# Kernel optimization log

Hardware: AMD Instinct MI355X
Metric: run time of the kernel (lower is better)

The kernel has to match this reference:

```python
import jax, jax.numpy as jnp
import numpy as np

N_NODES = 100000
N_EDGES = 3200000
D_IN = 128
D_HID = 16
N_CLS = 2


def gcn_conv(x, edge_index, W, b, n_nodes):
    """PyG GCNConv (normalize=True, add_self_loops=True, bias=True)."""
    h = x @ W  # [N, out]
    loop = jnp.arange(n_nodes, dtype=edge_index.dtype)
    src = jnp.concatenate([edge_index[0], loop])
    dst = jnp.concatenate([edge_index[1], loop])
    deg = jax.ops.segment_sum(jnp.ones_like(dst, dtype=h.dtype), dst, num_segments=n_nodes)
    dinv = jnp.where(deg > 0, jax.lax.rsqrt(deg), jnp.zeros_like(deg))
    norm = dinv[src] * dinv[dst]  # [E+N]
    msg = h[src] * norm[:, None]  # gather + scale
    out = jax.ops.segment_sum(msg, dst, num_segments=n_nodes)  # scatter-add
    return out + b


def setup_inputs() -> dict:
    key = jax.random.key(0)
    k1, k2, k3, k4, k5 = jax.random.split(key, 5)
    x = jax.random.normal(k1, (N_NODES, D_IN), dtype=jnp.float32)
    edge_index = jax.random.randint(k2, (2, N_EDGES), 0, N_NODES, dtype=jnp.int64)
    # Glorot-style init for GCNConv weights, zeros for bias (PyG default)
    W1 = jax.random.normal(k3, (D_IN, D_HID), dtype=jnp.float32) * (1.0 / np.sqrt(D_IN))
    b1 = jnp.zeros((D_HID,), dtype=jnp.float32)
    W2 = jax.random.normal(k4, (D_HID, N_CLS), dtype=jnp.float32) * (1.0 / np.sqrt(D_HID))
    b2 = jnp.zeros((N_CLS,), dtype=jnp.float32)
    return {"x": x, "edge_index": edge_index, "W1": W1, "b1": b1, "W2": W2, "b2": b2}


def reference(x, edge_index, W1, b1, W2, b2):
    n = x.shape[0]
    h = gcn_conv(x, edge_index, W1, b1, n)
    h = jax.nn.relu(h)
    # dropout is identity in eval mode
    h = gcn_conv(h, edge_index, W2, b2, n)
    return jax.nn.log_softmax(h, axis=1)
```

## Files before the change

kernel.cpp:

```cpp
#include <hip/hip_runtime.h>
#include <hip/hip_bf16.h>
#include <hip/hip_fp16.h>

#define D_IN  128
#define D_HID 16
#define N_CLS 2
#define NPB   256
#define MAXB  512
#define TILE  8192
#define XROW  136
#define LCAP  10496

#define FE 0

typedef short bf16x8 __attribute__((ext_vector_type(8)));
typedef float f32x4  __attribute__((ext_vector_type(4)));

__device__ __forceinline__ unsigned short f2bf(float f) {
    unsigned int u = __float_as_uint(f);
    u += 0x7FFFu + ((u >> 16) & 1u);
    return (unsigned short)(u >> 16);
}

template<bool I64>
__device__ __forceinline__ int lde(const void* p, size_t i) {
    if constexpr (I64) return (int)((const long long*)p)[i];
    else               return ((const int*)p)[i];
}

__global__ void k_detect(const int* __restrict__ ev, int* __restrict__ flags) {
    __shared__ int sE;
    if (threadIdx.x == 0) sE = 0;
    __syncthreads();
    if (ev[2 * threadIdx.x + 1] != 0) atomicOr(&sE, 1);
    __syncthreads();
    if (threadIdx.x == 0) flags[FE] = sE ? 0 : 1;
}

template<bool I64>
__device__ __forceinline__ void part_body(
        const void* __restrict__ ei, unsigned int* __restrict__ gcur,
        unsigned int* __restrict__ staged, int E, int cap,
        unsigned int* sbuf, unsigned short* bbuf,
        int* hist, int* lbase, int* gb, int* wsum) {
    int tid = threadIdx.x;
    int t0 = blockIdx.x * TILE;

    if (tid < MAXB) hist[tid] = 0;
    __syncthreads();

    int myB[8]; unsigned int myP[8]; int myR[8];
#pragma unroll
    for (int k = 0; k < 8; ++k) {
        int e = t0 + k * 1024 + tid;
        if (e < E) {
            int s = lde<I64>(ei, (size_t)e);
            int d = lde<I64>(ei, (size_t)E + e);
            int b = d >> 8;
            myB[k] = b;
            myP[k] = ((unsigned int)s << 8) | (unsigned int)(d & 255);
            myR[k] = atomicAdd(&hist[b], 1);
        } else myB[k] = -1;
    }
    __syncthreads();

    int lane = tid & 63, wv = tid >> 6;
    int v = 0, s = 0;
    if (tid < MAXB) {
        v = hist[tid];
        s = v;
#pragma unroll
        for (int m = 1; m < 64; m <<= 1) {
            int t = __shfl_up(s, m, 64);
            if (lane >= m) s += t;
        }
        if (lane == 63) wsum[wv] = s;
    }
    __syncthreads();
    if (tid < MAXB) {
        int woff = 0;
#pragma unroll
        for (int w = 0; w < 8; ++w) if (w < wv) woff += wsum[w];
        int excl = s + woff - v;
        lbase[tid] = excl;
        int gb_ = 0;
        if (v > 0) gb_ = (int)atomicAdd(&gcur[tid], (unsigned int)v);
        gb[tid] = gb_;
    }
    __syncthreads();

#pragma unroll
    for (int k = 0; k < 8; ++k) {
        if (myB[k] >= 0) {
            int pos = lbase[myB[k]] + myR[k];
            sbuf[pos] = myP[k];
            bbuf[pos] = (unsigned short)myB[k];
        }
    }
    __syncthreads();

    int tot = lbase[MAXB - 1] + hist[MAXB - 1];
    for (int i = tid; i < tot; i += 1024) {
        int b = bbuf[i];
        int rel = gb[b] + (i - lbase[b]);
        if (rel < cap)
            staged[(size_t)b * cap + rel] = sbuf[i];
    }
}

__global__ __launch_bounds__(1024) void k_part(
        const void* __restrict__ ei, unsigned int* __restrict__ gcur,
        unsigned int* __restrict__ staged, int E, int cap) {
    __shared__ unsigned int sbuf[TILE];
    __shared__ unsigned short bbuf[TILE];
    __shared__ int hist[MAXB], lbase[MAXB], gb[MAXB];
    __shared__ int wsum[8];
    __shared__ int sI64;
    int tid = threadIdx.x;
    if (tid == 0) sI64 = 1;
    __syncthreads();
    if (tid < 256 && 2 * tid + 1 < 2 * E && ((const int*)ei)[2 * tid + 1] != 0) sI64 = 0;
    __syncthreads();
    if (sI64) part_body<true >(ei, gcur, staged, E, cap, sbuf, bbuf, hist, lbase, gb, wsum);
    else      part_body<false>(ei, gcur, staged, E, cap, sbuf, bbuf, hist, lbase, gb, wsum);
}

__global__ __launch_bounds__(1024) void k_sortd(
        const unsigned int* __restrict__ staged, const unsigned int* __restrict__ gcur,
        unsigned int* __restrict__ staged2, unsigned int* __restrict__ dmeta,
        float* __restrict__ dinv, int cap, int N) {
    __shared__ unsigned int ebuf[LCAP];
    __shared__ unsigned int h[NPB];
    __shared__ unsigned int cur[NPB];
    __shared__ int wsum[4];
    int tid = threadIdx.x, b = blockIdx.x;
    long long s0 = (long long)b * cap;
    int cnt = (int)gcur[b];
    if (cnt > cap - NPB) cnt = cap - NPB;
    bool inL = cnt <= LCAP;
    if (tid < NPB) h[tid] = 0u;
    __syncthreads();
    for (int i = tid; i < cnt; i += 1024) {
        unsigned int p = staged[s0 + i];
        if (inL) ebuf[i] = p;
        atomicAdd(&h[p & 255], 1u);
    }
    __syncthreads();
    int v = 0, sIncl = 0;
    int lane = tid & 63, wv = tid >> 6;
    if (tid < NPB) {
        v = (int)h[tid];
        sIncl = v;
#pragma unroll
        for (int m = 1; m < 64; m <<= 1) {
            int t = __shfl_up(sIncl, m, 64);
            if (lane >= m) sIncl += t;
        }
        if (lane == 63) wsum[wv] = sIncl;
    }
    __syncthreads();
    if (tid < NPB) {
        int woff = 0;
#pragma unroll
        for (int w = 0; w < 4; ++w) if (w < wv) woff += wsum[w];
        int excl = sIncl + woff - v;
        int node = b * NPB + tid;
        int start = excl + tid;
        dmeta[node] = ((unsigned int)start << 16) | (unsigned int)v;
        cur[tid] = (unsigned int)start;
        if (node < N) dinv[node] = rsqrtf((float)(v + 1));
    }
    __syncthreads();
    for (int i = tid; i < cnt; i += 1024) {
        unsigned int p = inL ? ebuf[i] : staged[s0 + i];
        unsigned int r = atomicAdd(&cur[p & 255], 1u);
        staged2[s0 + r] = p;
    }
    __syncthreads();
    if (tid < NPB) {
        unsigned int pos = cur[tid];
        int node = b * NPB + tid;
        if ((int)pos < cap)
            staged2[s0 + pos] = ((unsigned int)node << 8) | (unsigned int)tid;
    }
}

__global__ __launch_bounds__(256) void k_gemm1m(
        const float* __restrict__ x, const float* __restrict__ W1,
        const float* __restrict__ dinv, __half* __restrict__ g1h, int n) {
    __shared__ short xhi[64 * XROW];
    __shared__ short xlo[64 * XROW];
    __shared__ short whi[16 * XROW];
    __shared__ short wlo[16 * XROW];
    int tid = threadIdx.x;
    int node0 = blockIdx.x * 64;

    for (int i = tid; i < D_IN * D_HID; i += 256) {
        int k = i >> 4, f = i & 15;
        float v = W1[i];
        unsigned short h = f2bf(v);
        float fh = __uint_as_float(((unsigned int)h) << 16);
        whi[f * XROW + k] = (short)h;
        wlo[f * XROW + k] = (short)f2bf(v - fh);
    }
    int limFlat = (n - node0) * D_IN;
#pragma unroll
    for (int it = 0; it < 8; ++it) {
        int flat = it * 1024 + tid * 4;
        float4 v = make_float4(0.f, 0.f, 0.f, 0.f);
        if (flat < limFlat) v = *(const float4*)(x + (size_t)node0 * D_IN + flat);
        int row = flat >> 7, k = flat & 127;
        unsigned int u0 = __float_as_uint(v.x), u1 = __float_as_uint(v.y);
        unsigned int u2 = __float_as_uint(v.z), u3 = __float_as_uint(v.w);
        unsigned short l0 = f2bf(v.x - __uint_as_float(u0 & 0xFFFF0000u));
        unsigned short l1 = f2bf(v.y - __uint_as_float(u1 & 0xFFFF0000u));
        unsigned short l2 = f2bf(v.z - __uint_as_float(u2 & 0xFFFF0000u));
        unsigned short l3 = f2bf(v.w - __uint_as_float(u3 & 0xFFFF0000u));
        int o = row * XROW + k;
        *(uint2*)(&xhi[o]) = make_uint2((u0 >> 16) | (u1 & 0xFFFF0000u),
                                        (u2 >> 16) | (u3 & 0xFFFF0000u));
        *(uint2*)(&xlo[o]) = make_uint2((unsigned int)l0 | ((unsigned int)l1 << 16),
                                        (unsigned int)l2 | ((unsigned int)l3 << 16));
    }
    __syncthreads();

    int w = tid >> 6, L = tid & 63;
    int m = L & 15, q = L >> 4;
    const short* axh = &xhi[(w * 16 + m) * XROW + q * 8];
    const short* axl = &xlo[(w * 16 + m) * XROW + q * 8];
    const short* bwh = &whi[m * XROW + q * 8];
    const short* bwl = &wlo[m * XROW + q * 8];
    f32x4 acc = {0.f, 0.f, 0.f, 0.f};
#pragma unroll
    for (int c = 0; c < 4; ++c) {
        bf16x8 ah = *(const bf16x8*)(axh + c * 32);
        bf16x8 al = *(const bf16x8*)(axl + c * 32);
        bf16x8 bh = *(const bf16x8*)(bwh + c * 32);
        bf16x8 bl = *(const bf16x8*)(bwl + c * 32);
        acc = __builtin_amdgcn_mfma_f32_16x16x32_bf16(ah, bh, acc, 0, 0, 0);
        acc = __builtin_amdgcn_mfma_f32_16x16x32_bf16(ah, bl, acc, 0, 0, 0);
        acc = __builtin_amdgcn_mfma_f32_16x16x32_bf16(al, bh, acc, 0, 0, 0);
    }
    int nodeB = node0 + w * 16 + q * 4;
#pragma unroll
    for (int r = 0; r < 4; ++r) {
        int node = nodeB + r;
        if (node < n) g1h[(size_t)node * D_HID + m] = __float2half(dinv[node] * acc[r]);
    }
}

__global__ __launch_bounds__(256) void k_agg1w(
        const unsigned int* __restrict__ staged2, const unsigned int* __restrict__ dmeta,
        const __half* __restrict__ g1h,
        const float* __restrict__ b1, const float* __restrict__ W2,
        float2* __restrict__ g2, int N, int cap) {
    int tid = threadIdx.x, b = blockIdx.x, by = blockIdx.y;
    long long s0 = (long long)b * cap;
    int lane = tid & 63;
    int f2 = lane & 7;
    int e8 = lane >> 3;
    int wid = (by << 2) + (tid >> 6);
    const __half2* g1h2 = (const __half2*)g1h;
    int f0 = f2 * 2;
    float b10 = b1[f0], b11 = b1[f0 + 1];
    float w00 = W2[f0 * N_CLS + 0], w01 = W2[f0 * N_CLS + 1];
    float w10 = W2[(f0 + 1) * N_CLS + 0], w11 = W2[(f0 + 1) * N_CLS + 1];
    unsigned int md[8];
#pragma unroll
    for (int k = 0; k < 8; ++k) md[k] = dmeta[b * NPB + wid + (k << 5)];
#pragma unroll 4
    for (int k = 0; k < 8; ++k) {
        int node = b * NPB + wid + (k << 5);
        const unsigned int* sp = staged2 + s0 + (md[k] >> 16);
        int cnt = (int)(md[k] & 0xFFFFu) + 1;
        float ax = 0.f, ay = 0.f;
        for (int base = 0; base < cnt; base += 64) {
            unsigned int pe[8];
#pragma unroll
            for (int j = 0; j < 8; ++j) {
                int idx = base + (j << 3) + e8;
                int c = idx < cnt ? idx : cnt - 1;
                pe[j] = sp[c];
            }
#pragma unroll
            for (int j = 0; j < 8; ++j) {
                int idx = base + (j << 3) + e8;
                float2 t = __half22float2(g1h2[(size_t)(pe[j] >> 8) * 8 + f2]);
                if (idx < cnt) { ax += t.x; ay += t.y; }
            }
        }
        ax += __shfl_xor(ax, 8, 64);  ay += __shfl_xor(ay, 8, 64);
        ax += __shfl_xor(ax, 16, 64); ay += __shfl_xor(ay, 16, 64);
        ax += __shfl_xor(ax, 32, 64); ay += __shfl_xor(ay, 32, 64);
        float di = rsqrtf((float)cnt);
        float r0 = fmaxf(b10 + di * ax, 0.f);
        float r1 = fmaxf(b11 + di * ay, 0.f);
        float c0 = r0 * w00 + r1 * w10;
        float c1 = r0 * w01 + r1 * w11;
        c0 += __shfl_xor(c0, 1, 64); c1 += __shfl_xor(c1, 1, 64);
        c0 += __shfl_xor(c0, 2, 64); c1 += __shfl_xor(c1, 2, 64);
        c0 += __shfl_xor(c0, 4, 64); c1 += __shfl_xor(c1, 4, 64);
        if (lane == 0 && node < N) g2[node] = make_float2(di * c0, di * c1);
    }
}

__global__ __launch_bounds__(256) void k_agg2w(
        const unsigned int* __restrict__ staged2, const unsigned int* __restrict__ dmeta,
        const float2* __restrict__ g2,
        const float* __restrict__ b2, float2* __restrict__ out, int N, int cap) {
    int tid = threadIdx.x, b = blockIdx.x, by = blockIdx.y;
    long long s0 = (long long)b * cap;
    int lane = tid & 63;
    int wid = (by << 2) + (tid >> 6);
    float bb0 = b2[0], bb1 = b2[1];
    unsigned int md[8];
#pragma unroll
    for (int k = 0; k < 8; ++k) md[k] = dmeta[b * NPB + wid + (k << 5)];
#pragma unroll 4
    for (int k = 0; k < 8; ++k) {
        int node = b * NPB + wid + (k << 5);
        const unsigned int* sp = staged2 + s0 + (md[k] >> 16);
        int cnt = (int)(md[k] & 0xFFFFu) + 1;
        float a0 = 0.f, a1 = 0.f;
        for (int base = 0; base < cnt; base += 64) {
            int idx = base + lane;
            int c = idx < cnt ? idx : cnt - 1;
            unsigned int p = sp[c];
            float2 t = g2[p >> 8];
            if (idx < cnt) { a0 += t.x; a1 += t.y; }
        }
#pragma unroll
        for (int mm = 1; mm < 64; mm <<= 1) {
            a0 += __shfl_xor(a0, mm, 64);
            a1 += __shfl_xor(a1, mm, 64);
        }
        if (lane == 0 && node < N) {
            float di = rsqrtf((float)cnt);
            float v0 = bb0 + di * a0;
            float v1 = bb1 + di * a1;
            float mx = fmaxf(v0, v1);
            float lse = mx + logf(expf(v0 - mx) + expf(v1 - mx));
            out[node] = make_float2(v0 - lse, v1 - lse);
        }
    }
}

__global__ void fb_deg_init(unsigned int* __restrict__ deg, int n) {
    int i = blockIdx.x * blockDim.x + threadIdx.x;
    if (i < n) deg[i] = 1u;
}
template<bool I64>
__global__ void fb_deg_count(const void* __restrict__ ei, unsigned int* __restrict__ deg,
                             int E, const int* __restrict__ flags) {
    if (flags[FE] != (int)I64) return;
    int e = blockIdx.x * blockDim.x + threadIdx.x;
    if (e < E) atomicAdd(&deg[lde<I64>(ei, (size_t)E + e)], 1u);
}
__global__ void fb_dinv_inplace(float* __restrict__ dinv, int n) {
    int i = blockIdx.x * blockDim.x + threadIdx.x;
    if (i < n) {
        unsigned int u = ((const unsigned int*)dinv)[i];
        dinv[i] = rsqrtf((float)u);
    }
}
__global__ void fb_a1_init(const float* __restrict__ h1, const float* __restrict__ dinv,
                           const float* __restrict__ b1, float* __restrict__ a1, int n) {
    int tid = blockIdx.x * blockDim.x + threadIdx.x;
    if (tid >= n * D_HID) return;
    int node = tid >> 4, f = tid & 15;
    float di = dinv[node];
    a1[tid] = b1[f] + di * di * h1[tid];
}
template<bool I64>
__global__ void fb_agg1(const void* __restrict__ ei, const float* __restrict__ dinv,
                        const float* __restrict__ h1, float* __restrict__ a1,
                        int E, const int* __restrict__ flags) {
    if (flags[FE] != (int)I64) return;
    int tid = blockIdx.x * blockDim.x + threadIdx.x;
    int e = tid >> 4, f = tid & 15;
    if (e >= E) return;
    int s = lde<I64>(ei, (size_t)e);
    int d = lde<I64>(ei, (size_t)E + e);
    float norm = dinv[s] * dinv[d];
    atomicAdd(&a1[(size_t)d * D_HID + f], h1[(size_t)s * D_HID + f] * norm);
}
__global__ void fb_relu_gemm2(const float* __restrict__ a1, const float* __restrict__ W2,
                              float* __restrict__ h2, int n) {
    int node = blockIdx.x * blockDim.x + threadIdx.x;
    if (node >= n) return;
    float c0 = 0.f, c1 = 0.f;
    const float* row = a1 + (size_t)node * D_HID;
#pragma unroll
    for (int f = 0; f < D_HID; ++f) {
        float r = fmaxf(row[f], 0.f);
        c0 += r * W2[f * N_CLS + 0];
        c1 += r * W2[f * N_CLS + 1];
    }
    h2[(size_t)node * 2 + 0] = c0;
    h2[(size_t)node * 2 + 1] = c1;
}
__global__ void fb_a2_init(const float* __restrict__ h2, const float* __restrict__ dinv,
                           const float* __restrict__ b2, float* __restrict__ a2, int n) {
    int tid = blockIdx.x * blockDim.x + threadIdx.x;
    if (tid >= n * N_CLS) return;
    int node = tid >> 1, c = tid & 1;
    float di = dinv[node];
    a2[tid] = b2[c] + di * di * h2[tid];
}
template<bool I64>
__global__ void fb_agg2(const void* __restrict__ ei, const float* __restrict__ dinv,
                        const float* __restrict__ h2, float* __restrict__ a2,
                        int E, const int* __restrict__ flags) {
    if (flags[FE] != (int)I64) return;
    int e = blockIdx.x * blockDim.x + threadIdx.x;
    if (e >= E) return;
    int s = lde<I64>(ei, (size_t)e);
    int d = lde<I64>(ei, (size_t)E + e);
    float norm = dinv[s] * dinv[d];
    atomicAdd(&a2[(size_t)d * 2 + 0], h2[(size_t)s * 2 + 0] * norm);
    atomicAdd(&a2[(size_t)d * 2 + 1], h2[(size_t)s * 2 + 1] * norm);
}
__global__ void fb_gemm1(const float* __restrict__ x, const float* __restrict__ W1,
                         float* __restrict__ h1, int n) {
    __shared__ float w[D_IN * D_HID];
    for (int i = threadIdx.x; i < D_IN * D_HID; i += blockDim.x) w[i] = W1[i];
    __syncthreads();
    int tid = blockIdx.x * blockDim.x + threadIdx.x;
    int node = tid >> 4, f = tid & 15;
    if (node >= n) return;
    const float4* xr = (const float4*)(x + (size_t)node * D_IN);
    float acc = 0.f;
#pragma unroll
    for (int k4 = 0; k4 < D_IN / 4; ++k4) {
        float4 v = xr[k4];
        int k = k4 * 4;
        acc += v.x * w[(k + 0) * D_HID + f];
        acc += v.y * w[(k + 1) * D_HID + f];
        acc += v.z * w[(k + 2) * D_HID + f];
        acc += v.w * w[(k + 3) * D_HID + f];
    }
    h1[tid] = acc;
}
__global__ void fb_lsm(const float* __restrict__ a2, float* __restrict__ out, int n) {
    int node = blockIdx.x * blockDim.x + threadIdx.x;
    if (node >= n) return;
    float v0 = a2[(size_t)node * 2 + 0];
    float v1 = a2[(size_t)node * 2 + 1];
    float m = fmaxf(v0, v1);
    float lse = m + logf(expf(v0 - m) + expf(v1 - m));
    out[(size_t)node * 2 + 0] = v0 - lse;
    out[(size_t)node * 2 + 1] = v1 - lse;
}

extern "C" void kernel_launch(void* const* d_in, const int* in_sizes, int n_in,
                              void* d_out, int out_size, void* d_ws, size_t ws_size,
                              hipStream_t stream) {
    const float* x  = (const float*)d_in[0];
    const void*  ei = d_in[1];
    const float* W1 = (const float*)d_in[2];
    const float* b1 = (const float*)d_in[3];
    const float* W2 = (const float*)d_in[4];
    const float* b2 = (const float*)d_in[5];

    const int N = in_sizes[0] / D_IN;
    const int E = in_sizes[1] / 2;
    const int nb = (N + NPB - 1) / NPB;

    int cap = ((2 * (E / nb + 1) + NPB) + 255) & ~255;
    if (cap < 1024) cap = 1024;

    const int B = 256;
    dim3 blk(B);
    const int nBlkN = (N + B - 1) / B;
    const int nBlkE = (E + B - 1) / B;
    char* ws = (char*)d_ws;

    auto al = [](size_t v) { return (v + 255) & ~(size_t)255; };
    const size_t oDinv   = 0;
    const size_t oDmeta  = al(oDinv + (size_t)N * 4);
    const size_t oGcur   = al(oDmeta + (size_t)nb * NPB * 4);
    const size_t oFlag   = al(oGcur + (size_t)MAXB * 4);
    const size_t oStage  = al(oFlag + 8);
    const size_t oStage2 = al(oStage + (size_t)nb * cap * 4);
    const size_t oG1h    = al(oStage2 + (size_t)nb * cap * 4);
    const size_t oG2     = al(oG1h + (size_t)N * D_HID * 2);
    const size_t needNew = al(oG2 + (size_t)N * 2 * 4);

    if (ws_size >= needNew && nb <= MAXB && cap <= 65280 && N < (1 << 24) - NPB) {
        float*        dinv    = (float*)(ws + oDinv);
        unsigned int* dmeta   = (unsigned int*)(ws + oDmeta);
        unsigned int* gcur    = (unsigned int*)(ws + oGcur);
        unsigned int* staged  = (unsigned int*)(ws + oStage);
        unsigned int* staged2 = (unsigned int*)(ws + oStage2);
        __half*       g1h     = (__half*)(ws + oG1h);
        float2*       g2      = (float2*)(ws + oG2);

        hipMemsetAsync(gcur, 0, (size_t)nb * 4, stream);

        dim3 gPart((E + TILE - 1) / TILE);
        k_part<<<gPart, dim3(1024), 0, stream>>>(ei, gcur, staged, E, cap);

        k_sortd<<<dim3(nb), dim3(1024), 0, stream>>>(staged, gcur, staged2, dmeta, dinv, cap, N);

        k_gemm1m<<<dim3((N + 63) / 64), dim3(256), 0, stream>>>(x, W1, dinv, g1h, N);

        k_agg1w<<<dim3(nb, 8), dim3(256), 0, stream>>>(staged2, dmeta, g1h, b1, W2, g2, N, cap);

        k_agg2w<<<dim3(nb, 8), dim3(256), 0, stream>>>(staged2, dmeta, g2, b2,
                                                       (float2*)d_out, N, cap);
    } else {
        float* dinv  = (float*)(ws + 0);
        float* h1    = (float*)(ws + 400128);
        float* a1    = (float*)(ws + 6800256);
        float* h2    = (float*)(ws + 13200384);
        float* a2    = (float*)(ws + 14000512);
        int*   flags = (int*)  (ws + 14800640);

        k_detect<<<dim3(1), blk, 0, stream>>>((const int*)ei, flags);
        fb_deg_init<<<dim3(nBlkN), blk, 0, stream>>>((unsigned int*)dinv, N);
        fb_deg_count<false><<<dim3(nBlkE), blk, 0, stream>>>(ei, (unsigned int*)dinv, E, flags);
        fb_deg_count<true ><<<dim3(nBlkE), blk, 0, stream>>>(ei, (unsigned int*)dinv, E, flags);
        fb_dinv_inplace<<<dim3(nBlkN), blk, 0, stream>>>(dinv, N);

        dim3 g_nh((N * D_HID + B - 1) / B);
        fb_gemm1<<<g_nh, blk, 0, stream>>>(x, W1, h1, N);
        fb_a1_init<<<g_nh, blk, 0, stream>>>(h1, dinv, b1, a1, N);
        dim3 g_eh(((size_t)E * D_HID + B - 1) / B);
        fb_agg1<false><<<g_eh, blk, 0, stream>>>(ei, dinv, h1, a1, E, flags);
        fb_agg1<true ><<<g_eh, blk, 0, stream>>>(ei, dinv, h1, a1, E, flags);
        fb_relu_gemm2<<<dim3(nBlkN), blk, 0, stream>>>(a1, W2, h2, N);
        dim3 g_n2((N * N_CLS + B - 1) / B);
        fb_a2_init<<<g_n2, blk, 0, stream>>>(h2, dinv, b2, a2, N);
        fb_agg2<false><<<dim3(nBlkE), blk, 0, stream>>>(ei, dinv, h2, a2, E, flags);
        fb_agg2<true ><<<dim3(nBlkE), blk, 0, stream>>>(ei, dinv, h2, a2, E, flags);
        fb_lsm<<<dim3(nBlkN), blk, 0, stream>>>(a2, (float*)d_out, N);
    }
}
```

Measured before the change: 213.0 us.

## Fuse per-bucket sort into layer-1 aggregation and count degrees in partition

Removes the separate k_sortd kernel. Degree counting moves into the partition kernel as global atomics on a zeroed deg array, and the GEMM computes dinv from it. The bucket counting sort and the layer-1 aggregation are fused into one 1024-thread block per bucket, which reads the sorted edges from LDS. This saves a launch and a pass over the staged edges. In exchange it adds 3.2M global atomics, and the aggregation runs with only nb blocks instead of nb×8, which lowers parallelism.

```diff
diff --git a/kernel.cpp b/kernel.cpp
--- a/kernel.cpp
+++ b/kernel.cpp
@@ -40,7 +40,8 @@
 template<bool I64>
 __device__ __forceinline__ void part_body(
         const void* __restrict__ ei, unsigned int* __restrict__ gcur,
-        unsigned int* __restrict__ staged, int E, int cap,
+        unsigned int* __restrict__ staged, unsigned int* __restrict__ deg,
+        int E, int cap,
         unsigned int* sbuf, unsigned short* bbuf,
         int* hist, int* lbase, int* gb, int* wsum) {
     int tid = threadIdx.x;
@@ -60,6 +61,7 @@
             myB[k] = b;
             myP[k] = ((unsigned int)s << 8) | (unsigned int)(d & 255);
             myR[k] = atomicAdd(&hist[b], 1);
+            atomicAdd(&deg[d], 1u);
         } else myB[k] = -1;
     }
     __syncthreads();
@@ -110,7 +112,8 @@
 
 __global__ __launch_bounds__(1024) void k_part(
         const void* __restrict__ ei, unsigned int* __restrict__ gcur,
-        unsigned int* __restrict__ staged, int E, int cap) {
+        unsigned int* __restrict__ staged, unsigned int* __restrict__ deg,
+        int E, int cap) {
     __shared__ unsigned int sbuf[TILE];
     __shared__ unsigned short bbuf[TILE];
     __shared__ int hist[MAXB], lbase[MAXB], gb[MAXB];
@@ -121,73 +124,13 @@
     __syncthreads();
     if (tid < 256 && 2 * tid + 1 < 2 * E && ((const int*)ei)[2 * tid + 1] != 0) sI64 = 0;
     __syncthreads();
-    if (sI64) part_body<true >(ei, gcur, staged, E, cap, sbuf, bbuf, hist, lbase, gb, wsum);
-    else      part_body<false>(ei, gcur, staged, E, cap, sbuf, bbuf, hist, lbase, gb, wsum);
-}
-
-__global__ __launch_bounds__(1024) void k_sortd(
-        const unsigned int* __restrict__ staged, const unsigned int* __restrict__ gcur,
-        unsigned int* __restrict__ staged2, unsigned int* __restrict__ dmeta,
-        float* __restrict__ dinv, int cap, int N) {
-    __shared__ unsigned int ebuf[LCAP];
-    __shared__ unsigned int h[NPB];
-    __shared__ unsigned int cur[NPB];
-    __shared__ int wsum[4];
-    int tid = threadIdx.x, b = blockIdx.x;
-    long long s0 = (long long)b * cap;
-    int cnt = (int)gcur[b];
-    if (cnt > cap - NPB) cnt = cap - NPB;
-    bool inL = cnt <= LCAP;
-    if (tid < NPB) h[tid] = 0u;
-    __syncthreads();
-    for (int i = tid; i < cnt; i += 1024) {
-        unsigned int p = staged[s0 + i];
-        if (inL) ebuf[i] = p;
-        atomicAdd(&h[p & 255], 1u);
-    }
-    __syncthreads();
-    int v = 0, sIncl = 0;
-    int lane = tid & 63, wv = tid >> 6;
-    if (tid < NPB) {
-        v = (int)h[tid];
-        sIncl = v;
-#pragma unroll
-        for (int m = 1; m < 64; m <<= 1) {
-            int t = __shfl_up(sIncl, m, 64);
-            if (lane >= m) sIncl += t;
-        }
-        if (lane == 63) wsum[wv] = sIncl;
-    }
-    __syncthreads();
-    if (tid < NPB) {
-        int woff = 0;
-#pragma unroll
-        for (int w = 0; w < 4; ++w) if (w < wv) woff += wsum[w];
-        int excl = sIncl + woff - v;
-        int node = b * NPB + tid;
-        int start = excl + tid;
-        dmeta[node] = ((unsigned int)start << 16) | (unsigned int)v;
-        cur[tid] = (unsigned int)start;
-        if (node < N) dinv[node] = rsqrtf((float)(v + 1));
-    }
-    __syncthreads();
-    for (int i = tid; i < cnt; i += 1024) {
-        unsigned int p = inL ? ebuf[i] : staged[s0 + i];
-        unsigned int r = atomicAdd(&cur[p & 255], 1u);
-        staged2[s0 + r] = p;
-    }
-    __syncthreads();
-    if (tid < NPB) {
-        unsigned int pos = cur[tid];
-        int node = b * NPB + tid;
-        if ((int)pos < cap)
-            staged2[s0 + pos] = ((unsigned int)node << 8) | (unsigned int)tid;
-    }
+    if (sI64) part_body<true >(ei, gcur, staged, deg, E, cap, sbuf, bbuf, hist, lbase, gb, wsum);
+    else      part_body<false>(ei, gcur, staged, deg, E, cap, sbuf, bbuf, hist, lbase, gb, wsum);
 }
 
 __global__ __launch_bounds__(256) void k_gemm1m(
         const float* __restrict__ x, const float* __restrict__ W1,
-        const float* __restrict__ dinv, __half* __restrict__ g1h, int n) {
+        const unsigned int* __restrict__ deg, __half* __restrict__ g1h, int n) {
     __shared__ short xhi[64 * XROW];
     __shared__ short xlo[64 * XROW];
     __shared__ short whi[16 * XROW];
@@ -245,54 +188,107 @@
 #pragma unroll
     for (int r = 0; r < 4; ++r) {
         int node = nodeB + r;
-        if (node < n) g1h[(size_t)node * D_HID + m] = __float2half(dinv[node] * acc[r]);
-    }
-}
-
-__global__ __launch_bounds__(256) void k_agg1w(
-        const unsigned int* __restrict__ staged2, const unsigned int* __restrict__ dmeta,
+        if (node < n) {
+            float di = rsqrtf((float)(deg[node] + 1u));
+            g1h[(size_t)node * D_HID + m] = __float2half(di * acc[r]);
+        }
+    }
+}
+
+__global__ __launch_bounds__(1024) void k_sagg1(
+        const unsigned int* __restrict__ staged, const unsigned int* __restrict__ gcur,
+        unsigned int* __restrict__ staged2, unsigned int* __restrict__ dmeta,
         const __half* __restrict__ g1h,
         const float* __restrict__ b1, const float* __restrict__ W2,
         float2* __restrict__ g2, int N, int cap) {
-    int tid = threadIdx.x, b = blockIdx.x, by = blockIdx.y;
+    __shared__ unsigned int ebuf[LCAP];
+    __shared__ unsigned int md[NPB];
+    __shared__ unsigned int cur[NPB];
+    __shared__ int wsum[4];
+    int tid = threadIdx.x, b = blockIdx.x;
     long long s0 = (long long)b * cap;
-    int lane = tid & 63;
-    int f2 = lane & 7;
-    int e8 = lane >> 3;
-    int wid = (by << 2) + (tid >> 6);
+    int cnt = (int)gcur[b];
+    if (cnt > cap - NPB) cnt = cap - NPB;
+    bool inL = (cnt + NPB) <= LCAP;
+
+    if (tid < NPB) cur[tid] = 0u;
+    __syncthreads();
+    for (int i = tid; i < cnt; i += 1024)
+        atomicAdd(&cur[staged[s0 + i] & 255], 1u);
+    __syncthreads();
+    int lane = tid & 63, wv = tid >> 6;
+    int v = 0, sIncl = 0;
+    if (tid < NPB) {
+        v = (int)cur[tid];
+        sIncl = v;
+#pragma unroll
+        for (int m = 1; m < 64; m <<= 1) {
+            int t = __shfl_up(sIncl, m, 64);
+            if (lane >= m) sIncl += t;
+        }
+        if (lane == 63) wsum[wv] = sIncl;
+    }
+    __syncthreads();
+    if (tid < NPB) {
+        int woff = 0;
+#pragma unroll
+        for (int w = 0; w < 4; ++w) if (w < wv) woff += wsum[w];
+        int start = (sIncl + woff - v) + tid;
+        md[tid] = ((unsigned int)start << 16) | (unsigned int)v;
+        cur[tid] = (unsigned int)start;
+    }
+    __syncthreads();
+    for (int i = tid; i < cnt; i += 1024) {
+        unsigned int p = staged[s0 + i];
+        unsigned int r = atomicAdd(&cur[p & 255], 1u);
+        staged2[s0 + r] = p;
+        if (inL) ebuf[r] = p;
+    }
+    __syncthreads();
+    if (tid < NPB) {
+        unsigned int pos = cur[tid];
+        int node = b * NPB + tid;
+        dmeta[node] = md[tid];
+        unsigned int sv = ((unsigned int)node << 8) | (unsigned int)tid;
+        if ((int)pos < cap) {
+            staged2[s0 + pos] = sv;
+            if (inL) ebuf[pos] = sv;
+        }
+    }
+    __syncthreads();
+
     const __half2* g1h2 = (const __half2*)g1h;
+    int f2 = lane & 7, e8 = lane >> 3;
     int f0 = f2 * 2;
     float b10 = b1[f0], b11 = b1[f0 + 1];
     float w00 = W2[f0 * N_CLS + 0], w01 = W2[f0 * N_CLS + 1];
     float w10 = W2[(f0 + 1) * N_CLS + 0], w11 = W2[(f0 + 1) * N_CLS + 1];
-    unsigned int md[8];
-#pragma unroll
-    for (int k = 0; k < 8; ++k) md[k] = dmeta[b * NPB + wid + (k << 5)];
-#pragma unroll 4
-    for (int k = 0; k < 8; ++k) {
-        int node = b * NPB + wid + (k << 5);
-        const unsigned int* sp = staged2 + s0 + (md[k] >> 16);
-        int cnt = (int)(md[k] & 0xFFFFu) + 1;
+#pragma unroll 2
+    for (int k = 0; k < 16; ++k) {
+        int dl = wv + (k << 4);
+        unsigned int m = md[dl];
+        int st = (int)(m >> 16);
+        int dcnt = (int)(m & 0xFFFFu) + 1;
         float ax = 0.f, ay = 0.f;
-        for (int base = 0; base < cnt; base += 64) {
+        for (int base = 0; base < dcnt; base += 64) {
             unsigned int pe[8];
 #pragma unroll
             for (int j = 0; j < 8; ++j) {
                 int idx = base + (j << 3) + e8;
-                int c = idx < cnt ? idx : cnt - 1;
-                pe[j] = sp[c];
+                int c = idx < dcnt ? idx : dcnt - 1;
+                pe[j] = inL ? ebuf[st + c] : staged2[s0 + st + c];
             }
 #pragma unroll
             for (int j = 0; j < 8; ++j) {
                 int idx = base + (j << 3) + e8;
                 float2 t = __half22float2(g1h2[(size_t)(pe[j] >> 8) * 8 + f2]);
-                if (idx < cnt) { ax += t.x; ay += t.y; }
+                if (idx < dcnt) { ax += t.x; ay += t.y; }
             }
         }
         ax += __shfl_xor(ax, 8, 64);  ay += __shfl_xor(ay, 8, 64);
         ax += __shfl_xor(ax, 16, 64); ay += __shfl_xor(ay, 16, 64);
         ax += __shfl_xor(ax, 32, 64); ay += __shfl_xor(ay, 32, 64);
-        float di = rsqrtf((float)cnt);
+        float di = rsqrtf((float)dcnt);
         float r0 = fmaxf(b10 + di * ax, 0.f);
         float r1 = fmaxf(b11 + di * ay, 0.f);
         float c0 = r0 * w00 + r1 * w10;
@@ -300,6 +296,7 @@
         c0 += __shfl_xor(c0, 1, 64); c1 += __shfl_xor(c1, 1, 64);
         c0 += __shfl_xor(c0, 2, 64); c1 += __shfl_xor(c1, 2, 64);
         c0 += __shfl_xor(c0, 4, 64); c1 += __shfl_xor(c1, 4, 64);
+        int node = b * NPB + dl;
         if (lane == 0 && node < N) g2[node] = make_float2(di * c0, di * c1);
     }
 }
@@ -476,35 +473,34 @@
     char* ws = (char*)d_ws;
 
     auto al = [](size_t v) { return (v + 255) & ~(size_t)255; };
-    const size_t oDinv   = 0;
-    const size_t oDmeta  = al(oDinv + (size_t)N * 4);
-    const size_t oGcur   = al(oDmeta + (size_t)nb * NPB * 4);
-    const size_t oFlag   = al(oGcur + (size_t)MAXB * 4);
-    const size_t oStage  = al(oFlag + 8);
+    const size_t oDeg    = 0;
+    const size_t oGcur   = al(oDeg + (size_t)N * 4);
+    const size_t zeroLen = al(oGcur + (size_t)MAXB * 4);
+    const size_t oDmeta  = zeroLen;
+    const size_t oStage  = al(oDmeta + (size_t)nb * NPB * 4);
     const size_t oStage2 = al(oStage + (size_t)nb * cap * 4);
     const size_t oG1h    = al(oStage2 + (size_t)nb * cap * 4);
     const size_t oG2     = al(oG1h + (size_t)N * D_HID * 2);
     const size_t needNew = al(oG2 + (size_t)N * 2 * 4);
 
     if (ws_size >= needNew && nb <= MAXB && cap <= 65280 && N < (1 << 24) - NPB) {
-        float*        dinv    = (float*)(ws + oDinv);
+        unsigned int* deg     = (unsigned int*)(ws + oDeg);
+        unsigned int* gcur    = (unsigned int*)(ws + oGcur);
         unsigned int* dmeta   = (unsigned int*)(ws + oDmeta);
-        unsigned int* gcur    = (unsigned int*)(ws + oGcur);
         unsigned int* staged  = (unsigned int*)(ws + oStage);
         unsigned int* staged2 = (unsigned int*)(ws + oStage2);
         __half*       g1h     = (__half*)(ws + oG1h);
         float2*       g2      = (float2*)(ws + oG2);
 
-        hipMemsetAsync(gcur, 0, (size_t)nb * 4, stream);
+        hipMemsetAsync(ws, 0, zeroLen, stream);
 
         dim3 gPart((E + TILE - 1) / TILE);
-        k_part<<<gPart, dim3(1024), 0, stream>>>(ei, gcur, staged, E, cap);
-
-        k_sortd<<<dim3(nb), dim3(1024), 0, stream>>>(staged, gcur, staged2, dmeta, dinv, cap, N);
-
-        k_gemm1m<<<dim3((N + 63) / 64), dim3(256), 0, stream>>>(x, W1, dinv, g1h, N);
-
-        k_agg1w<<<dim3(nb, 8), dim3(256), 0, stream>>>(staged2, dmeta, g1h, b1, W2, g2, N, cap);
+        k_part<<<gPart, dim3(1024), 0, stream>>>(ei, gcur, staged, deg, E, cap);
+
+        k_gemm1m<<<dim3((N + 63) / 64), dim3(256), 0, stream>>>(x, W1, deg, g1h, N);
+
+        k_sagg1<<<dim3(nb), dim3(1024), 0, stream>>>(staged, gcur, staged2, dmeta,
+                                                     g1h, b1, W2, g2, N, cap);
 
         k_agg2w<<<dim3(nb, 8), dim3(256), 0, stream>>>(staged2, dmeta, g2, b2,
                                                        (float2*)d_out, N, cap);
```

Result: slower. 337.0 us (+58.2%).
